# Kernel optimization log

Hardware: AMD Instinct MI355X
Metric: run time of the kernel (lower is better)

The kernel has to match this reference:

```python
import jax, jax.numpy as jnp
import numpy as np

B, N, DIM, H, K = 2, 8192, 256, 8, 32
HD = DIM // H


def setup_inputs() -> dict:
    key = jax.random.key(0)
    ks = jax.random.split(key, 10)
    s = 1.0 / np.sqrt(DIM)
    return {
        "x": jax.random.normal(ks[0], (B, N, DIM), jnp.float32),
        "xyz": jax.random.normal(ks[1], (B, N, 3), jnp.float32),
        "idx": jax.random.randint(ks[2], (B, N, K), 0, N, jnp.int32),
        "Wq": jax.random.normal(ks[3], (DIM, DIM), jnp.float32) * s,
        "bq": jnp.zeros((DIM,), jnp.float32),
        "Wk": jax.random.normal(ks[4], (DIM, DIM), jnp.float32) * s,
        "bk": jnp.zeros((DIM,), jnp.float32),
        "Wv": jax.random.normal(ks[5], (DIM, DIM), jnp.float32) * s,
        "bv": jnp.zeros((DIM,), jnp.float32),
        "Wo": jax.random.normal(ks[6], (DIM, DIM), jnp.float32) * s,
        "bo": jnp.zeros((DIM,), jnp.float32),
        "W1": jax.random.normal(ks[7], (3, 32), jnp.float32) * 0.5,
        "b1": jnp.zeros((32,), jnp.float32),
        "W2": jax.random.normal(ks[8], (32, H), jnp.float32) * 0.2,
        "b2": jnp.zeros((H,), jnp.float32),
    }


def reference(x, xyz, idx, Wq, bq, Wk, bk, Wv, bv, Wo, bo, W1, b1, W2, b2):
    Bn, Nn, C = x.shape
    k = idx.shape[-1]
    q = (x @ Wq + bq).reshape(Bn, Nn, H, HD)          # [B,N,H,hd]
    kf = (x @ Wk + bk).reshape(Bn, Nn, H, HD)
    vf = (x @ Wv + bv).reshape(Bn, Nn, H, HD)
    # gather k neighbors per point (per-batch fancy indexing)
    gather = jax.vmap(lambda f, i: f[i])               # [N,H,hd],[N,k] -> [N,k,H,hd]
    kn = gather(kf, idx)                               # [B,N,k,H,hd]
    vn = gather(vf, idx)
    nxyz = jax.vmap(lambda p, i: p[i])(xyz, idx)       # [B,N,k,3]
    rel = xyz[:, :, None, :] - nxyz                    # [B,N,k,3]
    bias = jax.nn.relu(rel @ W1 + b1) @ W2 + b2        # [B,N,k,H]
    scores = jnp.einsum('bnhd,bnkhd->bnhk', q, kn) / np.sqrt(HD).astype(np.float32)
    scores = scores + bias.transpose(0, 1, 3, 2)       # [B,N,H,k]
    attn = jax.nn.softmax(scores, axis=-1)
    out = jnp.einsum('bnhk,bnkhd->bnhd', attn, vn).reshape(Bn, Nn, C)
    return out @ Wo + bo
```

## Files before the change

### kernel.cpp

```cpp
#include <hip/hip_runtime.h>
#include <hip/hip_bf16.h>

typedef unsigned int uint32;
typedef unsigned short ushort;
typedef __attribute__((ext_vector_type(4))) float floatx4;
typedef __attribute__((ext_vector_type(8))) __bf16 bf16x8;

#define NPTS 8192
#define HSZ 524288

__device__ __forceinline__ ushort f2bf(float f) {
    uint32 u = __float_as_uint(f);
    uint32 r = (u + 0x7fffu + ((u >> 16) & 1u)) >> 16;
    return (ushort)r;
}
__device__ __forceinline__ float bf1(ushort u) { return __uint_as_float((uint32)u << 16); }
__device__ __forceinline__ float bflo(uint32 u) { return __uint_as_float(u << 16); }
__device__ __forceinline__ float bfhi(uint32 u) { return __uint_as_float(u & 0xffff0000u); }

__global__ __launch_bounds__(256) void prep_kernel(
    const float* __restrict__ x, const float* __restrict__ xyz, const int* __restrict__ idx,
    const float* __restrict__ Wq, const float* __restrict__ Wk,
    const float* __restrict__ Wv, const float* __restrict__ Wo,
    const float* __restrict__ bq, const float* __restrict__ bk, const float* __restrict__ bv,
    const float* __restrict__ W1, const float* __restrict__ b1,
    const float* __restrict__ W2, const float* __restrict__ b2,
    ushort* __restrict__ xb, ushort* __restrict__ Wqkvt, ushort* __restrict__ Wot,
    float* __restrict__ biasqkv, ushort* __restrict__ bias_hg) {
    const int bi = blockIdx.x;
    const int tid = threadIdx.x;
    if (bi < 4096) {
        int i = (bi * 256 + tid) * 4;
        float4 v = *(const float4*)(x + i);
        ushort4 o;
        o.x = f2bf(v.x); o.y = f2bf(v.y); o.z = f2bf(v.z); o.w = f2bf(v.w);
        *(ushort4*)(xb + i) = o;
    } else if (bi < 5120) {
        int f = (bi - 4096) * 256 + tid;
        if (f < 768 * 256) {
            int n = f >> 8, k = f & 255;
            int seg = n >> 8, nc = n & 255;
            const float* W = (seg == 0) ? Wq : (seg == 1) ? Wk : Wv;
            Wqkvt[f] = f2bf(W[k * 256 + nc]);
        } else {
            int g = f - 768 * 256;
            int n = g >> 8, k = g & 255;
            Wot[g] = f2bf(Wo[k * 256 + n]);
        }
        if (f < 768) biasqkv[f] = (f < 256) ? bq[f] : (f < 512) ? bk[f - 256] : bv[f - 512];
    } else {
        __shared__ float W1s[96], b1s[32], W2s[256], b2s[8];
        if (tid < 96) W1s[tid] = W1[tid];
        if (tid < 32) b1s[tid] = b1[tid];
        W2s[tid] = W2[tid];
        if (tid < 8) b2s[tid] = b2[tid];
        __syncthreads();
        const int wid = tid >> 6, lane = tid & 63;
        const int s = lane >> 5, j = lane & 31;
        const int p = (bi - 5120) * 8 + wid * 2 + s;
        const int b = p >> 13, n = p & 8191;
        const int nj = idx[(size_t)p * 32 + j];
        const size_t pb = ((size_t)b * NPTS + n) * 3;
        const size_t nb = ((size_t)b * NPTS + nj) * 3;
        const float rx = xyz[pb + 0] - xyz[nb + 0];
        const float ry = xyz[pb + 1] - xyz[nb + 1];
        const float rz = xyz[pb + 2] - xyz[nb + 2];
        float acc[8];
#pragma unroll
        for (int h = 0; h < 8; ++h) acc[h] = b2s[h];
#pragma unroll
        for (int u = 0; u < 32; ++u) {
            float hv = rx * W1s[u] + ry * W1s[32 + u] + rz * W1s[64 + u] + b1s[u];
            hv = fmaxf(hv, 0.f);
#pragma unroll
            for (int h = 0; h < 8; ++h) acc[h] += hv * W2s[u * 8 + h];
        }
#pragma unroll
        for (int h = 0; h < 8; ++h) bias_hg[(size_t)h * HSZ + p * 32 + j] = f2bf(acc[h]);
    }
}

__global__ __launch_bounds__(256) void gemm_qkv(const ushort* __restrict__ A,
                                                const ushort* __restrict__ Wt,
                                                const float* __restrict__ bias,
                                                ushort* __restrict__ qh, ushort* __restrict__ kh,
                                                ushort* __restrict__ vh) {
    __shared__ __align__(16) ushort As[128 * 64];
    __shared__ __align__(16) ushort Bs[128 * 64];
    const int tid = threadIdx.x;
    const int w = tid >> 6, lane = tid & 63;
    const int m0 = blockIdx.y * 128, n0 = blockIdx.x * 128;
    const int wm = (w & 1) * 64, wn = (w >> 1) * 64;

    floatx4 acc[4][4] = {};

    for (int kt = 0; kt < 256; kt += 64) {
        __syncthreads();
#pragma unroll
        for (int c4 = 0; c4 < 4; ++c4) {
            const int c = w * 4 + c4;
            const int r = c * 8 + (lane >> 3);
            const int gseg = (lane & 7) ^ (r & 7);
            const char* ga = (const char*)(A + (size_t)(m0 + r) * 256 + kt) + gseg * 16;
            const char* gb = (const char*)(Wt + (size_t)(n0 + r) * 256 + kt) + gseg * 16;
            __builtin_amdgcn_global_load_lds((const __attribute__((address_space(1))) void*)ga,
                                             (__attribute__((address_space(3))) void*)((char*)As + c * 1024),
                                             16, 0, 0);
            __builtin_amdgcn_global_load_lds((const __attribute__((address_space(1))) void*)gb,
                                             (__attribute__((address_space(3))) void*)((char*)Bs + c * 1024),
                                             16, 0, 0);
        }
        __syncthreads();

        bf16x8 af[2][4], bg[2][4];
#pragma unroll
        for (int kk = 0; kk < 2; ++kk) {
            const int s = kk * 4 + (lane >> 4);
            const int phys = s ^ (lane & 7);
#pragma unroll
            for (int i = 0; i < 4; ++i) {
                af[kk][i] = *(const bf16x8*)((const char*)As + (wm + i * 16 + (lane & 15)) * 128 + phys * 16);
                bg[kk][i] = *(const bf16x8*)((const char*)Bs + (wn + i * 16 + (lane & 15)) * 128 + phys * 16);
            }
        }
#pragma unroll
        for (int kk = 0; kk < 2; ++kk)
#pragma unroll
            for (int mi = 0; mi < 4; ++mi)
#pragma unroll
                for (int ni = 0; ni < 4; ++ni)
                    acc[mi][ni] = __builtin_amdgcn_mfma_f32_16x16x32_bf16(af[kk][mi], bg[kk][ni], acc[mi][ni], 0, 0, 0);
    }

#pragma unroll
    for (int ni = 0; ni < 4; ++ni) {
        const int col = n0 + wn + ni * 16 + (lane & 15);
        const int seg = col >> 8;
        const int head = (col >> 5) & 7;
        const int dim = col & 31;
        ushort* segp = (seg == 0) ? qh : (seg == 1) ? kh : vh;
        const float bv = bias[col];
#pragma unroll
        for (int mi = 0; mi < 4; ++mi) {
            const int row0 = m0 + wm + mi * 16 + (lane >> 4) * 4;
#pragma unroll
            for (int r = 0; r < 4; ++r)
                segp[(size_t)head * HSZ + (size_t)(row0 + r) * 32 + dim] = f2bf(acc[mi][ni][r] + bv);
        }
    }
}

__global__ __launch_bounds__(256) void gemm_mfma64(const ushort* __restrict__ A,
                                                   const ushort* __restrict__ Wt,
                                                   const float* __restrict__ bias,
                                                   float* __restrict__ outv, int N) {
    __shared__ __align__(16) ushort As[64 * 32];
    __shared__ __align__(16) ushort Bs[64 * 32];
    const int tid = threadIdx.x;
    const int w = tid >> 6, lane = tid & 63;
    const int m0 = blockIdx.y * 64, n0 = blockIdx.x * 64;
    const int row = tid >> 2;
    const int col16 = (tid & 3) * 16;

    floatx4 acc[4] = {};

    for (int kt = 0; kt < 256; kt += 32) {
        __syncthreads();
        {
            const char* ga = (const char*)(A + (size_t)(m0 + row) * 256 + kt) + col16;
            const char* gb = (const char*)(Wt + (size_t)(n0 + row) * 256 + kt) + col16;
            __builtin_amdgcn_global_load_lds((const __attribute__((address_space(1))) void*)ga,
                                             (__attribute__((address_space(3))) void*)((char*)As + w * 1024),
                                             16, 0, 0);
            __builtin_amdgcn_global_load_lds((const __attribute__((address_space(1))) void*)gb,
                                             (__attribute__((address_space(3))) void*)((char*)Bs + w * 1024),
                                             16, 0, 0);
        }
        __syncthreads();

        bf16x8 af = *(const bf16x8*)&As[(w * 16 + (lane & 15)) * 32 + (lane >> 4) * 8];
        bf16x8 bg[4];
#pragma unroll
        for (int ni = 0; ni < 4; ++ni)
            bg[ni] = *(const bf16x8*)&Bs[(ni * 16 + (lane & 15)) * 32 + (lane >> 4) * 8];
#pragma unroll
        for (int ni = 0; ni < 4; ++ni)
            acc[ni] = __builtin_amdgcn_mfma_f32_16x16x32_bf16(af, bg[ni], acc[ni], 0, 0, 0);
    }

#pragma unroll
    for (int ni = 0; ni < 4; ++ni) {
        const int col = n0 + ni * 16 + (lane & 15);
        const float bv = bias[col];
        const int row0 = m0 + w * 16 + (lane >> 4) * 4;
#pragma unroll
        for (int r = 0; r < 4; ++r)
            outv[(size_t)(row0 + r) * N + col] = acc[ni][r] + bv;
    }
}

__global__ __launch_bounds__(256) void attn_kernel(
    const ushort* __restrict__ qh, const ushort* __restrict__ kh, const ushort* __restrict__ vh,
    const int* __restrict__ idx, const ushort* __restrict__ bias_hg, ushort* __restrict__ out) {
    __shared__ __align__(16) float q_s[4][2][32];
    __shared__ __align__(8) uint2 oe_s[4][2][32];

    const int tid = threadIdx.x, wid = tid >> 6, lane = tid & 63;
    const int h = blockIdx.x >> 11;
    const int pg = blockIdx.x & 2047;
    const int pbase = pg * 8 + wid * 2;

    const char* kh_h = (const char*)(kh + (size_t)h * HSZ);
    const char* vh_h = (const char*)(vh + (size_t)h * HSZ);

    const int s = lane >> 5, j = lane & 31;
    const int p = pbase + s;
    const int b = p >> 13;

    const uint32 off = (uint32)(idx[(size_t)p * 32 + j] + b * NPTS) * 64u;
    oe_s[wid][s][j].x = off;
    q_s[wid][s][j] = bf1(qh[(size_t)h * HSZ + p * 32 + j]);

    float rinv;
    {
        const uint4* kp = (const uint4*)(kh_h + off);
        float d = 0.f;
#pragma unroll
        for (int c = 0; c < 4; ++c) {
            uint4 kv = kp[c];
            float4 qa = *(const float4*)&q_s[wid][s][c * 8];
            float4 qb = *(const float4*)&q_s[wid][s][c * 8 + 4];
            d += bflo(kv.x) * qa.x + bfhi(kv.x) * qa.y
               + bflo(kv.y) * qa.z + bfhi(kv.y) * qa.w
               + bflo(kv.z) * qb.x + bfhi(kv.z) * qb.y
               + bflo(kv.w) * qb.z + bfhi(kv.w) * qb.w;
        }
        const float sc = d * 0.17677669529663687f + bf1(bias_hg[(size_t)h * HSZ + p * 32 + j]);
        const float e = __expf(sc);
        oe_s[wid][s][j].y = __float_as_uint(e);
        float ssum = e;
#pragma unroll
        for (int msk = 16; msk >= 1; msk >>= 1) ssum += __shfl_xor(ssum, msk, 64);
        rinv = __builtin_amdgcn_rcpf(ssum);
    }

    {
        const int q4 = lane & 3, g = (lane >> 2) & 7;
        const char* vbase = vh_h + q4 * 16;
        float a0 = 0.f, a1 = 0.f, a2 = 0.f, a3 = 0.f, a4 = 0.f, a5 = 0.f, a6 = 0.f, a7 = 0.f;
#pragma unroll
        for (int i = 0; i < 4; ++i) {
            const uint2 oe = oe_s[wid][s][g * 4 + i];
            const float wgt = __uint_as_float(oe.y);
            const uint4 v = *(const uint4*)(vbase + oe.x);
            a0 += wgt * bflo(v.x); a1 += wgt * bfhi(v.x);
            a2 += wgt * bflo(v.y); a3 += wgt * bfhi(v.y);
            a4 += wgt * bflo(v.z); a5 += wgt * bfhi(v.z);
            a6 += wgt * bflo(v.w); a7 += wgt * bfhi(v.w);
        }
        const bool hi4 = (lane & 4) != 0;
        {
            float t0 = hi4 ? a0 : a4, t1 = hi4 ? a1 : a5, t2 = hi4 ? a2 : a6, t3 = hi4 ? a3 : a7;
            float k0 = hi4 ? a4 : a0, k1 = hi4 ? a5 : a1, k2 = hi4 ? a6 : a2, k3 = hi4 ? a7 : a3;
            a0 = k0 + __shfl_xor(t0, 4, 64);
            a1 = k1 + __shfl_xor(t1, 4, 64);
            a2 = k2 + __shfl_xor(t2, 4, 64);
            a3 = k3 + __shfl_xor(t3, 4, 64);
        }
        const bool hi8 = (lane & 8) != 0;
        {
            float t0 = hi8 ? a0 : a2, t1 = hi8 ? a1 : a3;
            float k0 = hi8 ? a2 : a0, k1 = hi8 ? a3 : a1;
            a0 = k0 + __shfl_xor(t0, 8, 64);
            a1 = k1 + __shfl_xor(t1, 8, 64);
        }
        const bool hi16 = (lane & 16) != 0;
        {
            float t0 = hi16 ? a0 : a1;
            float k0 = hi16 ? a1 : a0;
            a0 = k0 + __shfl_xor(t0, 16, 64);
        }
        const uint32 u = (uint32)f2bf(a0 * rinv);
        const uint32 up = (uint32)__shfl_xor((int)u, 16, 64);
        if (!hi16) {
            const int D = q4 * 8 + (hi4 ? 4 : 0) + (hi8 ? 2 : 0);
            *(uint32*)(out + (size_t)p * 256 + h * 32 + D) = u | (up << 16);
        }
    }
}

extern "C" void kernel_launch(void* const* d_in, const int* in_sizes, int n_in,
                              void* d_out, int out_size, void* d_ws, size_t ws_size,
                              hipStream_t stream) {
    const float* x   = (const float*)d_in[0];
    const float* xyz = (const float*)d_in[1];
    const int*   idx = (const int*)d_in[2];
    const float* Wq = (const float*)d_in[3];
    const float* bq = (const float*)d_in[4];
    const float* Wk = (const float*)d_in[5];
    const float* bk = (const float*)d_in[6];
    const float* Wv = (const float*)d_in[7];
    const float* bv = (const float*)d_in[8];
    const float* Wo = (const float*)d_in[9];
    const float* bo = (const float*)d_in[10];
    const float* W1 = (const float*)d_in[11];
    const float* b1 = (const float*)d_in[12];
    const float* W2 = (const float*)d_in[13];
    const float* b2 = (const float*)d_in[14];

    char* wsb = (char*)d_ws;
    ushort* x_bf    = (ushort*)wsb;
    ushort* aout_bf = x_bf;
    ushort* qh      = (ushort*)(wsb + 8388608);
    ushort* kh      = (ushort*)(wsb + 16777216);
    ushort* vh      = (ushort*)(wsb + 25165824);
    ushort* bias_hg = (ushort*)(wsb + 33554432);
    ushort* Wqkvt   = (ushort*)(wsb + 41943040);
    ushort* Wot     = (ushort*)(wsb + 42336256);
    float*  biasqkv = (float*)(wsb + 42467328);

    prep_kernel<<<7168, 256, 0, stream>>>(x, xyz, idx, Wq, Wk, Wv, Wo, bq, bk, bv,
                                          W1, b1, W2, b2, x_bf, Wqkvt, Wot, biasqkv, bias_hg);

    gemm_qkv<<<dim3(6, 128), 256, 0, stream>>>(x_bf, Wqkvt, biasqkv, qh, kh, vh);

    attn_kernel<<<16384, 256, 0, stream>>>(qh, kh, vh, idx, bias_hg, aout_bf);

    gemm_mfma64<<<dim3(4, 256), 256, 0, stream>>>(aout_bf, Wot, bo, (float*)d_out, 256);
}
```

Measured before the change: 181.0 us.

## Remap K-gather to V-gather lane layout and keep softmax weights in registers

The score phase previously had each lane read one neighbor's full 64-byte key row in four sequential 16-byte loads. Now each lane reads a 16-byte quarter of four neighbors, the same layout as the V phase, and reduces the dot products with two xor shuffles. The exp weights and neighbor offsets stay in registers rather than passing through shared memory, and the bias is staged through LDS. The aim is to issue more independent gather loads at once and remove the LDS round trip between the two phases, at the cost of extra shuffles.

After: 174.4 us. -3.6%, faster.

```diff
diff --git a/kernel.cpp b/kernel.cpp
--- a/kernel.cpp
+++ b/kernel.cpp
@@ -203,7 +203,8 @@
     const ushort* __restrict__ qh, const ushort* __restrict__ kh, const ushort* __restrict__ vh,
     const int* __restrict__ idx, const ushort* __restrict__ bias_hg, ushort* __restrict__ out) {
     __shared__ __align__(16) float q_s[4][2][32];
-    __shared__ __align__(8) uint2 oe_s[4][2][32];
+    __shared__ uint32 off_s[4][2][32];
+    __shared__ float bias_s[4][2][32];
 
     const int tid = threadIdx.x, wid = tid >> 6, lane = tid & 63;
     const int h = blockIdx.x >> 11;
@@ -217,42 +218,47 @@
     const int p = pbase + s;
     const int b = p >> 13;
 
-    const uint32 off = (uint32)(idx[(size_t)p * 32 + j] + b * NPTS) * 64u;
-    oe_s[wid][s][j].x = off;
+    off_s[wid][s][j] = (uint32)(idx[(size_t)p * 32 + j] + b * NPTS) * 64u;
     q_s[wid][s][j] = bf1(qh[(size_t)h * HSZ + p * 32 + j]);
-
-    float rinv;
+    bias_s[wid][s][j] = bf1(bias_hg[(size_t)h * HSZ + p * 32 + j]);
+
+    const int q4 = lane & 3, g = (lane >> 2) & 7;
+    const float4 qa = *(const float4*)&q_s[wid][s][q4 * 8];
+    const float4 qb = *(const float4*)&q_s[wid][s][q4 * 8 + 4];
+
+    uint32 off_r[4];
+#pragma unroll
+    for (int i = 0; i < 4; ++i) off_r[i] = off_s[wid][s][g * 4 + i];
+
+    float e_r[4];
+    float esum = 0.f;
+#pragma unroll
+    for (int i = 0; i < 4; ++i) {
+        const uint4 kv = *(const uint4*)(kh_h + off_r[i] + q4 * 16);
+        float d = bflo(kv.x) * qa.x + bfhi(kv.x) * qa.y
+                + bflo(kv.y) * qa.z + bfhi(kv.y) * qa.w
+                + bflo(kv.z) * qb.x + bfhi(kv.z) * qb.y
+                + bflo(kv.w) * qb.z + bfhi(kv.w) * qb.w;
+        d += __shfl_xor(d, 1, 64);
+        d += __shfl_xor(d, 2, 64);
+        const float sc = d * 0.17677669529663687f + bias_s[wid][s][g * 4 + i];
+        const float e = __expf(sc);
+        e_r[i] = e;
+        esum += e;
+    }
+    float ssum = esum;
+    ssum += __shfl_xor(ssum, 4, 64);
+    ssum += __shfl_xor(ssum, 8, 64);
+    ssum += __shfl_xor(ssum, 16, 64);
+    const float rinv = __builtin_amdgcn_rcpf(ssum);
+
     {
-        const uint4* kp = (const uint4*)(kh_h + off);
-        float d = 0.f;
-#pragma unroll
-        for (int c = 0; c < 4; ++c) {
-            uint4 kv = kp[c];
-            float4 qa = *(const float4*)&q_s[wid][s][c * 8];
-            float4 qb = *(const float4*)&q_s[wid][s][c * 8 + 4];
-            d += bflo(kv.x) * qa.x + bfhi(kv.x) * qa.y
-               + bflo(kv.y) * qa.z + bfhi(kv.y) * qa.w
-               + bflo(kv.z) * qb.x + bfhi(kv.z) * qb.y
-               + bflo(kv.w) * qb.z + bfhi(kv.w) * qb.w;
-        }
-        const float sc = d * 0.17677669529663687f + bf1(bias_hg[(size_t)h * HSZ + p * 32 + j]);
-        const float e = __expf(sc);
-        oe_s[wid][s][j].y = __float_as_uint(e);
-        float ssum = e;
-#pragma unroll
-        for (int msk = 16; msk >= 1; msk >>= 1) ssum += __shfl_xor(ssum, msk, 64);
-        rinv = __builtin_amdgcn_rcpf(ssum);
-    }
-
-    {
-        const int q4 = lane & 3, g = (lane >> 2) & 7;
         const char* vbase = vh_h + q4 * 16;
         float a0 = 0.f, a1 = 0.f, a2 = 0.f, a3 = 0.f, a4 = 0.f, a5 = 0.f, a6 = 0.f, a7 = 0.f;
 #pragma unroll
         for (int i = 0; i < 4; ++i) {
-            const uint2 oe = oe_s[wid][s][g * 4 + i];
-            const float wgt = __uint_as_float(oe.y);
-            const uint4 v = *(const uint4*)(vbase + oe.x);
+            const float wgt = e_r[i];
+            const uint4 v = *(const uint4*)(vbase + off_r[i]);
             a0 += wgt * bflo(v.x); a1 += wgt * bfhi(v.x);
             a2 += wgt * bflo(v.y); a3 += wgt * bfhi(v.y);
             a4 += wgt * bflo(v.z); a5 += wgt * bfhi(v.z);
```
